# Kernel optimization log

Measured on AMD Instinct MI355X. Metric: run time of the kernel, lower is better.

## Reference

```python
import jax, jax.numpy as jnp
import numpy as np

N = 100000   # nodes
E = 3200000  # edges (avg degree 32)
D = 2        # spatial dim (2D collective motion)
C = 1.0      # spring constant c
R_C = 1.0    # rest length r_c
P = 2        # potential exponent p
GAMMA = 0.1  # damping gamma
EPS = 1e-12  # torch F.normalize eps


def setup_inputs() -> dict:
    key = jax.random.key(0)
    k1, k2, k3, k4 = jax.random.split(key, 4)
    x = jax.random.normal(k1, (N, D), dtype=jnp.float32) * 10.0  # positions
    v = jax.random.normal(k2, (N, D), dtype=jnp.float32)          # velocities
    src = jax.random.randint(k3, (E,), 0, N)                      # edge sources
    dst = jax.random.randint(k4, (E,), 0, N)                      # edge destinations
    return {"x": x, "v": v, "src": src, "dst": dst}


def reference(x, v, src, dst):
    # calc_message: dr = dst_pos - src_pos (non-periodic euclid distance)
    dr = x[dst] - x[src]                                   # [E, D]
    abs_dr = jnp.linalg.norm(dr, axis=-1, keepdims=True)   # [E, 1]
    unit_dr = dr / jnp.maximum(abs_dr, EPS)                # F.normalize
    force = -C * P * (abs_dr - R_C) ** (P - 1)             # spring force magnitude
    m = force * unit_dr                                    # [E, D] message
    # update_all: fn.sum of messages at dst nodes -> acceleration
    a = jax.ops.segment_sum(m, dst, num_segments=N)        # [N, D]
    # damping term
    return a - GAMMA * v
```

## Files before the change

### kernel.cpp

```cpp
#include <hip/hip_runtime.h>

#define GAMMA 0.1f
#define EPS_F 1e-12f

#define S_NODES 20000
#define SCAN_THREADS 1024
#define B_TARGET 51

#define EDGE(dd, ss) do {                                        \
    int d_ = (dd);                                               \
    if (d_ >= lo && d_ < hi) {                                   \
        float2 xs = x[(ss)];                                     \
        float2 xd = x[d_];                                       \
        float dx = xd.x - xs.x;                                  \
        float dy = xd.y - xs.y;                                  \
        float r = sqrtf(dx * dx + dy * dy);                      \
        float sc = -2.0f * (r - 1.0f) / fmaxf(r, EPS_F);         \
        atomicAdd(&acc[d_ - lo].x, sc * dx);                     \
        atomicAdd(&acc[d_ - lo].y, sc * dy);                     \
    }                                                            \
} while (0)

__global__ __launch_bounds__(SCAN_THREADS, 1)
void scan_kernel(const float2* __restrict__ x,
                 const int4* __restrict__ src4,
                 const int4* __restrict__ dst4,
                 const int* __restrict__ src,
                 const int* __restrict__ dst,
                 float2* __restrict__ ws,
                 int e, int n, int B, int chunk) {
    __shared__ float2 acc[S_NODES];
    int p = blockIdx.x / B;
    int b = blockIdx.x - p * B;
    int lo = p * S_NODES;
    int hi = min(lo + S_NODES, n);
    int tid = threadIdx.x;

    for (int i = tid; i < S_NODES; i += SCAN_THREADS)
        acc[i] = make_float2(0.f, 0.f);
    __syncthreads();

    int estart = b * chunk;
    int eend = min(estart + chunk, e);
    if (estart < eend) {
        int nvec = (eend - estart) >> 2;
        const int4* d4p = dst4 + (estart >> 2);
        const int4* s4p = src4 + (estart >> 2);
        int nvec2 = nvec >> 1;
        for (int i = tid; i < nvec2; i += SCAN_THREADS) {
            int4 da = d4p[i];
            int4 sa = s4p[i];
            int4 db = d4p[i + nvec2];
            int4 sb = s4p[i + nvec2];
            EDGE(da.x, sa.x);
            EDGE(da.y, sa.y);
            EDGE(da.z, sa.z);
            EDGE(da.w, sa.w);
            EDGE(db.x, sb.x);
            EDGE(db.y, sb.y);
            EDGE(db.z, sb.z);
            EDGE(db.w, sb.w);
        }
        for (int i = (nvec2 << 1) + tid; i < nvec; i += SCAN_THREADS) {
            int4 d4 = d4p[i];
            int4 s4 = s4p[i];
            EDGE(d4.x, s4.x);
            EDGE(d4.y, s4.y);
            EDGE(d4.z, s4.z);
            EDGE(d4.w, s4.w);
        }
        for (int i = estart + (nvec << 2) + tid; i < eend; i += SCAN_THREADS)
            EDGE(dst[i], src[i]);
    }
    __syncthreads();

    float2* wsb = ws + (size_t)blockIdx.x * S_NODES;
    for (int i = tid; i < S_NODES; i += SCAN_THREADS)
        wsb[i] = acc[i];
}

__global__ __launch_bounds__(256)
void reduce_kernel(const float2* __restrict__ ws,
                   const float2* __restrict__ v,
                   float2* __restrict__ out,
                   int n, int B) {
    int i = blockIdx.x * blockDim.x + threadIdx.x;
    if (i >= n) return;
    int p = i / S_NODES;
    int loc = i - p * S_NODES;
    const float2* base = ws + ((size_t)(p * B) * S_NODES + loc);
    float sx0 = 0.f, sy0 = 0.f, sx1 = 0.f, sy1 = 0.f;
    float sx2 = 0.f, sy2 = 0.f, sx3 = 0.f, sy3 = 0.f;
    int b = 0;
    for (; b + 8 <= B; b += 8) {
        float2 t0 = base[(size_t)(b + 0) * S_NODES];
        float2 t1 = base[(size_t)(b + 1) * S_NODES];
        float2 t2 = base[(size_t)(b + 2) * S_NODES];
        float2 t3 = base[(size_t)(b + 3) * S_NODES];
        float2 t4 = base[(size_t)(b + 4) * S_NODES];
        float2 t5 = base[(size_t)(b + 5) * S_NODES];
        float2 t6 = base[(size_t)(b + 6) * S_NODES];
        float2 t7 = base[(size_t)(b + 7) * S_NODES];
        sx0 += t0.x; sy0 += t0.y; sx1 += t1.x; sy1 += t1.y;
        sx2 += t2.x; sy2 += t2.y; sx3 += t3.x; sy3 += t3.y;
        sx0 += t4.x; sy0 += t4.y; sx1 += t5.x; sy1 += t5.y;
        sx2 += t6.x; sy2 += t6.y; sx3 += t7.x; sy3 += t7.y;
    }
    for (; b < B; ++b) {
        float2 t = base[(size_t)b * S_NODES];
        sx0 += t.x; sy0 += t.y;
    }
    float sx = (sx0 + sx1) + (sx2 + sx3);
    float sy = (sy0 + sy1) + (sy2 + sy3);
    float2 vi = v[i];
    out[i] = make_float2(sx - GAMMA * vi.x, sy - GAMMA * vi.y);
}

__global__ void init_out_kernel(const float2* __restrict__ v,
                                float2* __restrict__ out, int n) {
    int i = blockIdx.x * blockDim.x + threadIdx.x;
    if (i < n) {
        float2 vi = v[i];
        out[i] = make_float2(-GAMMA * vi.x, -GAMMA * vi.y);
    }
}

__device__ __forceinline__ void do_edge_atomic(const float2* __restrict__ x,
                                               int s, int d,
                                               float* __restrict__ out) {
    float2 xs = x[s];
    float2 xd = x[d];
    float dx = xd.x - xs.x;
    float dy = xd.y - xs.y;
    float r = sqrtf(dx * dx + dy * dy);
    float sc = -2.0f * (r - 1.0f) / fmaxf(r, EPS_F);
    atomicAdd(&out[2 * d], sc * dx);
    atomicAdd(&out[2 * d + 1], sc * dy);
}

__global__ void edge_kernel_atomic(const float2* __restrict__ x,
                                   const int4* __restrict__ src4,
                                   const int4* __restrict__ dst4,
                                   const int* __restrict__ src,
                                   const int* __restrict__ dst,
                                   float* __restrict__ out,
                                   int e4, int e_total) {
    int i = blockIdx.x * blockDim.x + threadIdx.x;
    if (i < e4) {
        int4 s = src4[i];
        int4 d = dst4[i];
        do_edge_atomic(x, s.x, d.x, out);
        do_edge_atomic(x, s.y, d.y, out);
        do_edge_atomic(x, s.z, d.z, out);
        do_edge_atomic(x, s.w, d.w, out);
    }
    if (i == 0) {
        for (int e = e4 * 4; e < e_total; ++e)
            do_edge_atomic(x, src[e], dst[e], out);
    }
}

extern "C" void kernel_launch(void* const* d_in, const int* in_sizes, int n_in,
                              void* d_out, int out_size, void* d_ws, size_t ws_size,
                              hipStream_t stream) {
    const float2* x = (const float2*)d_in[0];
    const float2* v = (const float2*)d_in[1];
    const int* src  = (const int*)d_in[2];
    const int* dst  = (const int*)d_in[3];

    int n = in_sizes[0] / 2;
    int e = in_sizes[2];

    float* out = (float*)d_out;

    int P = (n + S_NODES - 1) / S_NODES;
    size_t per_b = (size_t)P * S_NODES * sizeof(float2);
    int Bmax = (per_b > 0) ? (int)(ws_size / per_b) : 0;
    int B = B_TARGET < Bmax ? B_TARGET : Bmax;

    if (B >= 1) {
        int chunk = (((e + B - 1) / B) + 3) & ~3;
        scan_kernel<<<P * B, SCAN_THREADS, 0, stream>>>(
            x, (const int4*)src, (const int4*)dst, src, dst,
            (float2*)d_ws, e, n, B, chunk);
        int threads = 256;
        reduce_kernel<<<(n + threads - 1) / threads, threads, 0, stream>>>(
            (const float2*)d_ws, v, (float2*)out, n, B);
    } else {
        int threads = 256;
        init_out_kernel<<<(n + threads - 1) / threads, threads, 0, stream>>>(
            v, (float2*)out, n);
        int e4 = e / 4;
        int blocks = (e4 + threads - 1) / threads;
        if (blocks < 1) blocks = 1;
        edge_kernel_atomic<<<blocks, threads, 0, stream>>>(
            x, (const int4*)src, (const int4*)dst, src, dst, out, e4, e);
    }
}
```

Measured before the change: 127.7 us.

## Fuse scan and reduce into cooperative kernel, split LDS accumulators, use rsq

Measured after the change: 294.7 us. +130.7%, slower.

```diff
diff --git a/kernel.cpp b/kernel.cpp
--- a/kernel.cpp
+++ b/kernel.cpp
@@ -1,4 +1,7 @@
 #include <hip/hip_runtime.h>
+#include <hip/hip_cooperative_groups.h>
+
+namespace cg = cooperative_groups;
 
 #define GAMMA 0.1f
 #define EPS_F 1e-12f
@@ -6,6 +9,120 @@
 #define S_NODES 20000
 #define SCAN_THREADS 1024
 #define B_TARGET 51
+
+#define EDGE_S(dd, ss) do {                                      \
+    int d_ = (dd);                                               \
+    if (d_ >= lo && d_ < hi) {                                   \
+        float2 xs = x[(ss)];                                     \
+        float2 xd = x[d_];                                       \
+        float dx = xd.x - xs.x;                                  \
+        float dy = xd.y - xs.y;                                  \
+        float d2 = dx * dx + dy * dy;                            \
+        float ir = d2 > 0.f ? __builtin_amdgcn_rsqf(d2) : 0.f;   \
+        float sc = 2.f * ir - 2.f;                               \
+        atomicAdd(&accx[d_ - lo], sc * dx);                      \
+        atomicAdd(&accy[d_ - lo], sc * dy);                      \
+    }                                                            \
+} while (0)
+
+__global__ __launch_bounds__(SCAN_THREADS, 1)
+void fused_kernel(const float2* __restrict__ x,
+                  const int4* __restrict__ src4,
+                  const int4* __restrict__ dst4,
+                  const int* __restrict__ src,
+                  const int* __restrict__ dst,
+                  const float2* __restrict__ v,
+                  float2* __restrict__ ws,
+                  float2* __restrict__ out,
+                  int e, int n, int B, int chunk) {
+    __shared__ float accx[S_NODES];
+    __shared__ float accy[S_NODES];
+    int p = blockIdx.x / B;
+    int b = blockIdx.x - p * B;
+    int lo = p * S_NODES;
+    int hi = min(lo + S_NODES, n);
+    int tid = threadIdx.x;
+
+    for (int i = tid; i < S_NODES; i += SCAN_THREADS) {
+        accx[i] = 0.f;
+        accy[i] = 0.f;
+    }
+    __syncthreads();
+
+    int estart = b * chunk;
+    int eend = min(estart + chunk, e);
+    if (estart < eend) {
+        int nvec = (eend - estart) >> 2;
+        const int4* d4p = dst4 + (estart >> 2);
+        const int4* s4p = src4 + (estart >> 2);
+        int nvec2 = nvec >> 1;
+        for (int i = tid; i < nvec2; i += SCAN_THREADS) {
+            int4 da = d4p[i];
+            int4 sa = s4p[i];
+            int4 db = d4p[i + nvec2];
+            int4 sb = s4p[i + nvec2];
+            EDGE_S(da.x, sa.x);
+            EDGE_S(da.y, sa.y);
+            EDGE_S(da.z, sa.z);
+            EDGE_S(da.w, sa.w);
+            EDGE_S(db.x, sb.x);
+            EDGE_S(db.y, sb.y);
+            EDGE_S(db.z, sb.z);
+            EDGE_S(db.w, sb.w);
+        }
+        for (int i = (nvec2 << 1) + tid; i < nvec; i += SCAN_THREADS) {
+            int4 d4 = d4p[i];
+            int4 s4 = s4p[i];
+            EDGE_S(d4.x, s4.x);
+            EDGE_S(d4.y, s4.y);
+            EDGE_S(d4.z, s4.z);
+            EDGE_S(d4.w, s4.w);
+        }
+        for (int i = estart + (nvec << 2) + tid; i < eend; i += SCAN_THREADS)
+            EDGE_S(dst[i], src[i]);
+    }
+    __syncthreads();
+
+    float2* wsb = ws + (size_t)blockIdx.x * S_NODES;
+    for (int i = tid; i < S_NODES; i += SCAN_THREADS)
+        wsb[i] = make_float2(accx[i], accy[i]);
+
+    __threadfence();
+    cg::this_grid().sync();
+
+    int gsz = (int)(gridDim.x * SCAN_THREADS);
+    for (int i = (int)blockIdx.x * SCAN_THREADS + tid; i < n; i += gsz) {
+        int pp = i / S_NODES;
+        int loc = i - pp * S_NODES;
+        const float2* base = ws + ((size_t)(pp * B) * S_NODES + loc);
+        float sx0 = 0.f, sy0 = 0.f, sx1 = 0.f, sy1 = 0.f;
+        float sx2 = 0.f, sy2 = 0.f, sx3 = 0.f, sy3 = 0.f;
+        int bb = 0;
+        for (; bb + 8 <= B; bb += 8) {
+            float2 t0 = base[(size_t)(bb + 0) * S_NODES];
+            float2 t1 = base[(size_t)(bb + 1) * S_NODES];
+            float2 t2 = base[(size_t)(bb + 2) * S_NODES];
+            float2 t3 = base[(size_t)(bb + 3) * S_NODES];
+            float2 t4 = base[(size_t)(bb + 4) * S_NODES];
+            float2 t5 = base[(size_t)(bb + 5) * S_NODES];
+            float2 t6 = base[(size_t)(bb + 6) * S_NODES];
+            float2 t7 = base[(size_t)(bb + 7) * S_NODES];
+            sx0 += t0.x; sy0 += t0.y; sx1 += t1.x; sy1 += t1.y;
+            sx2 += t2.x; sy2 += t2.y; sx3 += t3.x; sy3 += t3.y;
+            sx0 += t4.x; sy0 += t4.y; sx1 += t5.x; sy1 += t5.y;
+            sx2 += t6.x; sy2 += t6.y; sx3 += t7.x; sy3 += t7.y;
+        }
+        for (; bb < B; ++bb) {
+            float2 t = base[(size_t)bb * S_NODES];
+            sx0 += t.x; sy0 += t.y;
+        }
+        float sx = (sx0 + sx1) + (sx2 + sx3);
+        float sy = (sy0 + sy1) + (sy2 + sy3);
+        float2 vi = v[i];
+        out[i] = make_float2(sx - GAMMA * vi.x, sy - GAMMA * vi.y);
+    }
+}
+
 
 #define EDGE(dd, ss) do {                                        \
     int d_ = (dd);                                               \
@@ -14,10 +131,11 @@
         float2 xd = x[d_];                                       \
         float dx = xd.x - xs.x;                                  \
         float dy = xd.y - xs.y;                                  \
-        float r = sqrtf(dx * dx + dy * dy);                      \
-        float sc = -2.0f * (r - 1.0f) / fmaxf(r, EPS_F);         \
-        atomicAdd(&acc[d_ - lo].x, sc * dx);                     \
-        atomicAdd(&acc[d_ - lo].y, sc * dy);                     \
+        float d2 = dx * dx + dy * dy;                            \
+        float ir = d2 > 0.f ? __builtin_amdgcn_rsqf(d2) : 0.f;   \
+        float sc = 2.f * ir - 2.f;                               \
+        atomicAdd(&accx[d_ - lo], sc * dx);                      \
+        atomicAdd(&accy[d_ - lo], sc * dy);                      \
     }                                                            \
 } while (0)
 
@@ -29,15 +147,18 @@
                  const int* __restrict__ dst,
                  float2* __restrict__ ws,
                  int e, int n, int B, int chunk) {
-    __shared__ float2 acc[S_NODES];
+    __shared__ float accx[S_NODES];
+    __shared__ float accy[S_NODES];
     int p = blockIdx.x / B;
     int b = blockIdx.x - p * B;
     int lo = p * S_NODES;
     int hi = min(lo + S_NODES, n);
     int tid = threadIdx.x;
 
-    for (int i = tid; i < S_NODES; i += SCAN_THREADS)
-        acc[i] = make_float2(0.f, 0.f);
+    for (int i = tid; i < S_NODES; i += SCAN_THREADS) {
+        accx[i] = 0.f;
+        accy[i] = 0.f;
+    }
     __syncthreads();
 
     int estart = b * chunk;
@@ -76,7 +197,7 @@
 
     float2* wsb = ws + (size_t)blockIdx.x * S_NODES;
     for (int i = tid; i < S_NODES; i += SCAN_THREADS)
-        wsb[i] = acc[i];
+        wsb[i] = make_float2(accx[i], accy[i]);
 }
 
 __global__ __launch_bounds__(256)
@@ -171,29 +292,44 @@
     int n = in_sizes[0] / 2;
     int e = in_sizes[2];
 
-    float* out = (float*)d_out;
+    float2* out = (float2*)d_out;
+    float2* ws  = (float2*)d_ws;
 
     int P = (n + S_NODES - 1) / S_NODES;
     size_t per_b = (size_t)P * S_NODES * sizeof(float2);
     int Bmax = (per_b > 0) ? (int)(ws_size / per_b) : 0;
     int B = B_TARGET < Bmax ? B_TARGET : Bmax;
+    if (P >= 1 && B > 256 / P) B = 256 / P;
 
     if (B >= 1) {
         int chunk = (((e + B - 1) / B) + 3) & ~3;
-        scan_kernel<<<P * B, SCAN_THREADS, 0, stream>>>(
-            x, (const int4*)src, (const int4*)dst, src, dst,
-            (float2*)d_ws, e, n, B, chunk);
+        int grid = P * B;
+
+        const int4* src4 = (const int4*)src;
+        const int4* dst4 = (const int4*)dst;
+        void* args[] = { (void*)&x, (void*)&src4, (void*)&dst4,
+                         (void*)&src, (void*)&dst, (void*)&v,
+                         (void*)&ws, (void*)&out,
+                         (void*)&e, (void*)&n, (void*)&B, (void*)&chunk };
+        hipError_t err = hipLaunchCooperativeKernel(
+            (const void*)fused_kernel, dim3(grid), dim3(SCAN_THREADS),
+            args, 0, stream);
+        if (err == hipSuccess) return;
+
+        scan_kernel<<<grid, SCAN_THREADS, 0, stream>>>(
+            x, src4, dst4, src, dst, ws, e, n, B, chunk);
         int threads = 256;
         reduce_kernel<<<(n + threads - 1) / threads, threads, 0, stream>>>(
-            (const float2*)d_ws, v, (float2*)out, n, B);
+            ws, v, out, n, B);
     } else {
         int threads = 256;
         init_out_kernel<<<(n + threads - 1) / threads, threads, 0, stream>>>(
-            v, (float2*)out, n);
+            v, out, n);
         int e4 = e / 4;
         int blocks = (e4 + threads - 1) / threads;
         if (blocks < 1) blocks = 1;
         edge_kernel_atomic<<<blocks, threads, 0, stream>>>(
-            x, (const int4*)src, (const int4*)dst, src, dst, out, e4, e);
-    }
-}
+            x, (const int4*)src, (const int4*)dst, src, dst,
+            (float*)d_out, e4, e);
+    }
+}
```
